# Kernel tuning notes

Hardware: AMD Instinct MI355X
Metric: run time of the kernel (lower is better)

The kernel has to match this reference:

```python
import jax, jax.numpy as jnp
import numpy as np

B, M, K, F_IN, H = 64, 1024, 16, 4, 64  # B graphs of M nodes each, k=16 neighbors


def _knn_idx(h):
    # h: [B, M, H] -> indices of K nearest neighbors (excluding self): [B, M, K]
    sq = jnp.sum(h * h, axis=-1)                                   # [B, M]
    d = sq[:, :, None] + sq[:, None, :] - 2.0 * jnp.einsum('bmf,bnf->bmn', h, h)
    d = jnp.where(jnp.eye(M, dtype=bool)[None], jnp.float32(jnp.inf), d)
    _, idx = jax.lax.top_k(-d, K)                                  # smallest distances
    return idx


def _edge_conv(h, w1, b1, w2, b2):
    # Dynamic-graph EdgeConv with max aggregation (PyG default):
    # msg = MLP(concat[x_i, x_j - x_i]); out_i = max_j msg
    idx = _knn_idx(h)                                              # [B, M, K]
    x_j = jax.vmap(lambda hb, ib: hb[ib])(h, idx)                  # [B, M, K, H]
    x_i = jnp.broadcast_to(h[:, :, None, :], x_j.shape)
    msg = jnp.concatenate([x_i, x_j - x_i], axis=-1)               # [B, M, K, 2H]
    msg = jax.nn.relu(msg @ w1 + b1) @ w2 + b2                     # [B, M, K, H]
    return jnp.max(msg, axis=2)                                    # [B, M, H]


def setup_inputs() -> dict:
    key = jax.random.key(0)
    ks = jax.random.split(key, 20)

    def lin(k, fi, fo):
        return jax.random.normal(k, (fi, fo), jnp.float32) / np.sqrt(fi)

    inp = {
        'x': jax.random.normal(ks[0], (B * M, F_IN), jnp.float32),
        'batch': jnp.repeat(jnp.arange(B, dtype=jnp.int64), M),
        # encoder: Linear(4,32) ReLU Linear(32,64) ReLU
        'enc_w1': lin(ks[1], F_IN, 32), 'enc_b1': jnp.zeros((32,), jnp.float32),
        'enc_w2': lin(ks[2], 32, H),    'enc_b2': jnp.zeros((H,), jnp.float32),
        # EdgeConv MLPs: Linear(128,64) ReLU Linear(64,64)
        'ec1_w1': lin(ks[3], 2 * H, H), 'ec1_b1': jnp.zeros((H,), jnp.float32),
        'ec1_w2': lin(ks[4], H, H),     'ec1_b2': jnp.zeros((H,), jnp.float32),
        'ec2_w1': lin(ks[5], 2 * H, H), 'ec2_b1': jnp.zeros((H,), jnp.float32),
        'ec2_w2': lin(ks[6], H, H),     'ec2_b2': jnp.zeros((H,), jnp.float32),
        # output MLP: Linear(64,32) ReLU Linear(32,1)
        'out_w1': lin(ks[7], H, 32),    'out_b1': jnp.zeros((32,), jnp.float32),
        'out_w2': lin(ks[8], 32, 1),    'out_b2': jnp.zeros((1,), jnp.float32),
    }
    return inp


def reference(x, batch, enc_w1, enc_b1, enc_w2, enc_b2,
              ec1_w1, ec1_b1, ec1_w2, ec1_b2,
              ec2_w1, ec2_b1, ec2_w2, ec2_b2,
              out_w1, out_b1, out_w2, out_b2):
    # batch is repeat(arange(B), M): equal-size graphs -> reshape into [B, M, .]
    h = jax.nn.relu(jax.nn.relu(x @ enc_w1 + enc_b1) @ enc_w2 + enc_b2)  # [N, 64]
    h = h.reshape(B, M, H)
    h = _edge_conv(h, ec1_w1, ec1_b1, ec1_w2, ec1_b2)
    h = _edge_conv(h, ec2_w1, ec2_b1, ec2_w2, ec2_b2)
    g = jnp.mean(h, axis=1)                                        # global_mean_pool -> [B, 64]
    out = jax.nn.relu(g @ out_w1 + out_b1) @ out_w2 + out_b2       # [B, 1]
    return out.reshape(-1)                                         # [B]
```

## Files before the change

### kernel.cpp

```cpp
#include <hip/hip_runtime.h>
#include <math.h>

#define B_ 64
#define M_ 1024
#define H_ 64
#define N_ (B_*M_)

typedef _Float16 half8 __attribute__((ext_vector_type(8)));
typedef float  floatx4 __attribute__((ext_vector_type(4)));

#define MFMA16(a,b,c) __builtin_amdgcn_mfma_f32_16x16x32_f16(a,b,c,0,0,0)
#define MED3(a,b,c)   __builtin_amdgcn_fmed3f(a,b,c)

__global__ __launch_bounds__(256) void enc_kernel(
    const float* __restrict__ x,
    const float* __restrict__ w1,
    const float* __restrict__ b1,
    const float* __restrict__ w2,
    const float* __restrict__ b2,
    float* __restrict__ h,
    _Float16* __restrict__ hhi,
    _Float16* __restrict__ hlo,
    float* __restrict__ sq)
{
    __shared__ float sw1[4*32];
    __shared__ float sb1[32];
    __shared__ float sw2[32*64];
    __shared__ float sb2[64];
    int t = threadIdx.x;
    for (int i = t; i < 128; i += 256) sw1[i] = w1[i];
    if (t < 32) sb1[t] = b1[t];
    for (int i = t; i < 2048; i += 256) sw2[i] = w2[i];
    if (t < 64) sb2[t] = b2[t];
    __syncthreads();
    int n = blockIdx.x * 256 + t;
    float4 xv = *(const float4*)(x + (size_t)n*4);
    float hid[32];
    #pragma unroll
    for (int o = 0; o < 32; ++o) {
        float a = sb1[o] + xv.x*sw1[0*32+o] + xv.y*sw1[1*32+o]
                        + xv.z*sw1[2*32+o] + xv.w*sw1[3*32+o];
        hid[o] = fmaxf(a, 0.f);
    }
    float* hout = h + (size_t)n*64;
    float sqa = 0.f;
    #pragma unroll 4
    for (int oc = 0; oc < 16; ++oc) {
        float4 acc = make_float4(sb2[oc*4+0], sb2[oc*4+1], sb2[oc*4+2], sb2[oc*4+3]);
        #pragma unroll
        for (int f = 0; f < 32; ++f) {
            float4 w = *(const float4*)(sw2 + f*64 + oc*4);
            float hv = hid[f];
            acc.x += hv*w.x; acc.y += hv*w.y; acc.z += hv*w.z; acc.w += hv*w.w;
        }
        acc.x = fmaxf(acc.x,0.f); acc.y = fmaxf(acc.y,0.f);
        acc.z = fmaxf(acc.z,0.f); acc.w = fmaxf(acc.w,0.f);
        *(float4*)(hout + oc*4) = acc;
        sqa += acc.x*acc.x + acc.y*acc.y + acc.z*acc.z + acc.w*acc.w;
        union { _Float16 f[4]; uint2 u; } Hh, Hl;
        Hh.f[0]=(_Float16)acc.x; Hh.f[1]=(_Float16)acc.y;
        Hh.f[2]=(_Float16)acc.z; Hh.f[3]=(_Float16)acc.w;
        Hl.f[0]=(_Float16)(acc.x-(float)Hh.f[0]); Hl.f[1]=(_Float16)(acc.y-(float)Hh.f[1]);
        Hl.f[2]=(_Float16)(acc.z-(float)Hh.f[2]); Hl.f[3]=(_Float16)(acc.w-(float)Hh.f[3]);
        *(uint2*)(hhi + (size_t)n*64 + oc*4) = Hh.u;
        *(uint2*)(hlo + (size_t)n*64 + oc*4) = Hl.u;
    }
    sq[n] = sqa;
}

__global__ __launch_bounds__(256) void convert_kernel(
    const float* __restrict__ h,
    _Float16* __restrict__ hhi, _Float16* __restrict__ hlo,
    float* __restrict__ sq)
{
    int t = threadIdx.x, lane = t & 63, w = t >> 6;
    int base = blockIdx.x * 64 + w * 16;
    for (int it = 0; it < 16; ++it) {
        int i = base + it;
        float v = h[(size_t)i*64 + lane];
        _Float16 hi = (_Float16)v;
        _Float16 lo = (_Float16)(v - (float)hi);
        hhi[(size_t)i*64 + lane] = hi;
        hlo[(size_t)i*64 + lane] = lo;
        float s = v*v;
        #pragma unroll
        for (int off = 1; off < 64; off <<= 1) s += __shfl_xor(s, off, 64);
        if (lane == 0) sq[i] = s;
    }
}

__global__ __launch_bounds__(256) void gemmA_kernel(
    const float* __restrict__ h,
    const float* __restrict__ w1,
    float* __restrict__ A)
{
    __shared__ float sw[64*64];
    int t = threadIdx.x;
    for (int idx = t; idx < 4096; idx += 256) sw[idx] = w1[4096 + idx];
    __syncthreads();
    int n = blockIdx.x * 256 + t;
    float4 hv[16];
    const float* src = h + (size_t)n*64;
    #pragma unroll
    for (int c = 0; c < 16; ++c) hv[c] = *(const float4*)(src + c*4);
    float* dst = A + (size_t)n*64;
    #pragma unroll 2
    for (int oc = 0; oc < 16; ++oc) {
        float4 acc = make_float4(0.f,0.f,0.f,0.f);
        #pragma unroll
        for (int f = 0; f < 64; ++f) {
            float xv = ((const float*)hv)[f];
            float4 w = *(const float4*)(sw + f*64 + oc*4);
            acc.x += xv*w.x; acc.y += xv*w.y; acc.z += xv*w.z; acc.w += xv*w.w;
        }
        *(float4*)(dst + oc*4) = acc;
    }
}

__global__ __launch_bounds__(256) void knn_kernel(
    const _Float16* __restrict__ hhi,
    const _Float16* __restrict__ hlo,
    const float* __restrict__ sqg,
    unsigned short* __restrict__ knn)
{
    __shared__ float D[4][64*33];
    __shared__ float sqS[1024];
    int t = threadIdx.x, lane = t & 63, w = t >> 6;
    int bi = blockIdx.x;
    int g  = (bi & 7) | ((bi >> 7) << 3);
    int qt = (bi >> 3) & 15;
    const _Float16* hhig = hhi + (size_t)g*M_*64;
    const _Float16* hlog = hlo + (size_t)g*M_*64;
    const float*    sqb  = sqg + (size_t)g*M_;
    ((float4*)sqS)[t] = ((const float4*)sqb)[t];

    int m16  = lane & 15;
    int koct = (lane >> 4) * 8;
    half8 Ahi[4][2], Alo[4][2];
    #pragma unroll
    for (int rb = 0; rb < 4; ++rb) {
        const _Float16* ph = hhig + (size_t)(qt*64 + rb*16 + m16)*64;
        const _Float16* pl = hlog + (size_t)(qt*64 + rb*16 + m16)*64;
        Ahi[rb][0] = *(const half8*)(ph + koct);
        Ahi[rb][1] = *(const half8*)(ph + 32 + koct);
        Alo[rb][0] = *(const half8*)(pl + koct);
        Alo[rb][1] = *(const half8*)(pl + 32 + koct);
    }
    float* Dw   = D[w];
    int    crow = (lane >> 4) * 4;
    float  bd[16];
    #pragma unroll
    for (int k = 0; k < 16; ++k) bd[k] = INFINITY;
    int cand0 = w*256;
    __syncthreads();
    float c1 = 1.f + sqS[qt*64 + lane];
    int selfc_all = qt*64 + lane;

    #pragma unroll
    for (int cc = 0; cc < 8; ++cc) {
        int cbase = cand0 + cc*32;
        half8 Bhi[2][2], Blo[2][2];
        #pragma unroll
        for (int cb = 0; cb < 2; ++cb) {
            const _Float16* ph = hhig + (size_t)(cbase + cb*16 + m16)*64;
            const _Float16* pl = hlog + (size_t)(cbase + cb*16 + m16)*64;
            Bhi[cb][0] = *(const half8*)(ph + koct);
            Bhi[cb][1] = *(const half8*)(ph + 32 + koct);
            Blo[cb][0] = *(const half8*)(pl + koct);
            Blo[cb][1] = *(const half8*)(pl + 32 + koct);
        }
        #pragma unroll
        for (int rb = 0; rb < 4; ++rb) {
            #pragma unroll
            for (int cb = 0; cb < 2; ++cb) {
                floatx4 acc = {0.f, 0.f, 0.f, 0.f};
                acc = MFMA16(Ahi[rb][0], Bhi[cb][0], acc);
                acc = MFMA16(Ahi[rb][1], Bhi[cb][1], acc);
                acc = MFMA16(Ahi[rb][0], Blo[cb][0], acc);
                acc = MFMA16(Ahi[rb][1], Blo[cb][1], acc);
                acc = MFMA16(Alo[rb][0], Bhi[cb][0], acc);
                acc = MFMA16(Alo[rb][1], Bhi[cb][1], acc);
                #pragma unroll
                for (int r = 0; r < 4; ++r)
                    Dw[(rb*16 + crow + r)*33 + cb*16 + m16] = acc[r];
            }
        }
        const float* drow = Dw + lane*33;
        int selfc = selfc_all - cbase;
        #pragma unroll
        for (int c8 = 0; c8 < 4; ++c8) {
            float sv[8], qv[8];
            #pragma unroll
            for (int j = 0; j < 8; ++j) {
                sv[j] = drow[c8*8 + j];
                qv[j] = sqS[cbase + c8*8 + j];
            }
            #pragma unroll
            for (int j = 0; j < 8; ++j) {
                int c = c8*8 + j;
                float s  = fmaf(-2.f, sv[j], qv[j]);
                float t2 = c1 + s;
                unsigned kb = (__float_as_uint(t2) & 0xFFFFFC00u)
                            | (unsigned)(cbase + c);
                float fk = __uint_as_float(kb);
                if (c == selfc) fk = INFINITY;
                float nb0 = fminf(bd[0], fk);
                #pragma unroll
                for (int k = 15; k >= 1; --k) bd[k] = MED3(fk, bd[k-1], bd[k]);
                bd[0] = nb0;
            }
        }
    }

    __syncthreads();
    float* md = &D[0][0];
    #pragma unroll
    for (int k = 0; k < 16; ++k) md[lane*65 + w*16 + k] = bd[k];
    __syncthreads();
    if (w == 0) {
        float b2[16];
        #pragma unroll
        for (int k = 0; k < 16; ++k) b2[k] = INFINITY;
        const float* mrow = md + lane*65;
        #pragma unroll
        for (int c8 = 0; c8 < 8; ++c8) {
            float sv[8];
            #pragma unroll
            for (int j = 0; j < 8; ++j) sv[j] = mrow[c8*8 + j];
            #pragma unroll
            for (int j = 0; j < 8; ++j) {
                float s = sv[j];
                float nb0 = fminf(b2[0], s);
                #pragma unroll
                for (int k = 15; k >= 1; --k) b2[k] = MED3(s, b2[k-1], b2[k]);
                b2[0] = nb0;
            }
        }
        union { unsigned short us[16]; uint4 v4[2]; } o;
        #pragma unroll
        for (int k = 0; k < 16; ++k)
            o.us[k] = (unsigned short)(__float_as_uint(b2[k]) & 1023u);
        size_t gq = (size_t)g*M_ + qt*64 + lane;
        uint4* dst = (uint4*)(knn + gq*16);
        dst[0] = o.v4[0];
        dst[1] = o.v4[1];
    }
}

__global__ __launch_bounds__(256) void edge_kernel(
    const float* __restrict__ h,
    const float* __restrict__ A,
    const unsigned short* __restrict__ knn,
    const float* __restrict__ w1,
    const float* __restrict__ b1,
    const float* __restrict__ w2,
    const float* __restrict__ b2,
    float* __restrict__ hout)
{
    __shared__ __align__(16) _Float16 wdf[16*64*8];
    __shared__ __align__(16) _Float16 w2f[16*64*8];
    float* CsB = (float*)w2f;
    int t = threadIdx.x;
    for (int u = t; u < 512; u += 256) {
        int ulane = u & 63, nt = u >> 7, ks = (u >> 6) & 1;
        int n = nt*16 + (ulane & 15);
        int kbase = ks*32 + ((ulane >> 4) * 8);
        int fh = (((nt*2+ks)*2+0)*64 + ulane)*8;
        int fl = (((nt*2+ks)*2+1)*64 + ulane)*8;
        #pragma unroll
        for (int j = 0; j < 8; ++j) {
            int k = kbase + j;
            float vd = w1[k*64+n] - w1[4096 + k*64+n];
            _Float16 dh = (_Float16)vd;
            wdf[fh+j] = dh;
            wdf[fl+j] = (_Float16)(vd - (float)dh);
            float v2 = w2[k*64+n];
            _Float16 h2 = (_Float16)v2;
            w2f[fh+j] = h2;
            w2f[fl+j] = (_Float16)(v2 - (float)h2);
        }
    }
    __syncthreads();
    int lane = t & 63, wid = t >> 6;
    int m16 = lane & 15, gid = lane >> 4;
    int koct = gid*8, crow = gid*4;
    int bi = blockIdx.x;
    int g  = (bi & 7) | ((bi >> 7) << 3);
    int qt = (bi >> 3) & 15;
    int i0 = g*M_ + qt*64 + wid*16;
    const float* Ab = A + (size_t)g*M_*H_;

    half8 W2r[4][2][2];
    #pragma unroll
    for (int nt = 0; nt < 4; ++nt)
        #pragma unroll
        for (int ks = 0; ks < 2; ++ks)
            #pragma unroll
            for (int p = 0; p < 2; ++p)
                W2r[nt][ks][p] = *(const half8*)&w2f[(((nt*2+ks)*2+p)*64+lane)*8];

    float b1v[4];
    #pragma unroll
    for (int nt = 0; nt < 4; ++nt) b1v[nt] = b1[nt*16+m16];
    float b2v = b2[gid*16+m16];
    __syncthreads();

    half8 Hh[2], Hl[2];
    #pragma unroll
    for (int ks = 0; ks < 2; ++ks) {
        const float* hp = h + (size_t)(i0+m16)*64 + ks*32 + koct;
        float4 v0 = *(const float4*)hp;
        float4 v1 = *(const float4*)(hp+4);
        float va[8] = {v0.x,v0.y,v0.z,v0.w,v1.x,v1.y,v1.z,v1.w};
        #pragma unroll
        for (int j = 0; j < 8; ++j) {
            _Float16 hi = (_Float16)va[j];
            Hh[ks][j] = hi;
            Hl[ks][j] = (_Float16)(va[j]-(float)hi);
        }
    }
    #pragma unroll
    for (int nt = 0; nt < 4; ++nt) {
        floatx4 acc = {b1v[nt], b1v[nt], b1v[nt], b1v[nt]};
        #pragma unroll
        for (int ks = 0; ks < 2; ++ks) {
            half8 wh = *(const half8*)&wdf[(((nt*2+ks)*2+0)*64+lane)*8];
            half8 wl = *(const half8*)&wdf[(((nt*2+ks)*2+1)*64+lane)*8];
            acc = MFMA16(Hh[ks], wh, acc);
            acc = MFMA16(Hh[ks], wl, acc);
            acc = MFMA16(Hl[ks], wh, acc);
        }
        #pragma unroll
        for (int r = 0; r < 4; ++r)
            CsB[((wid*16) + crow + r)*64 + nt*16 + m16] = acc[r];
    }
    __syncthreads();

    const unsigned short* knb = knn + (size_t)i0*16;
    #pragma unroll 2
    for (int nn = 0; nn < 16; ++nn) {
        int j = knb[nn*16 + m16];
        const float* Ap = Ab + (size_t)j*64;
        half8 Mh[2], Ml[2];
        #pragma unroll
        for (int ks = 0; ks < 2; ++ks) {
            float4 a0 = *(const float4*)(Ap + ks*32 + koct);
            float4 a1 = *(const float4*)(Ap + ks*32 + koct + 4);
            const float* cp = &CsB[(wid*16 + nn)*64 + ks*32 + koct];
            float4 c0 = *(const float4*)cp;
            float4 c1 = *(const float4*)(cp+4);
            float mv[8] = {
                fmaxf(a0.x+c0.x,0.f), fmaxf(a0.y+c0.y,0.f),
                fmaxf(a0.z+c0.z,0.f), fmaxf(a0.w+c0.w,0.f),
                fmaxf(a1.x+c1.x,0.f), fmaxf(a1.y+c1.y,0.f),
                fmaxf(a1.z+c1.z,0.f), fmaxf(a1.w+c1.w,0.f)};
            #pragma unroll
            for (int jj = 0; jj < 8; ++jj) {
                _Float16 hi = (_Float16)mv[jj];
                Mh[ks][jj] = hi;
                Ml[ks][jj] = (_Float16)(mv[jj]-(float)hi);
            }
        }
        floatx4 acc[4];
        #pragma unroll
        for (int nt = 0; nt < 4; ++nt) {
            acc[nt] = (floatx4){0.f,0.f,0.f,0.f};
            #pragma unroll
            for (int ks = 0; ks < 2; ++ks) {
                acc[nt] = MFMA16(Mh[ks], W2r[nt][ks][0], acc[nt]);
                acc[nt] = MFMA16(Mh[ks], W2r[nt][ks][1], acc[nt]);
                acc[nt] = MFMA16(Ml[ks], W2r[nt][ks][0], acc[nt]);
            }
        }
        float om[4];
        #pragma unroll
        for (int nt = 0; nt < 4; ++nt) {
            float mr = fmaxf(fmaxf(acc[nt][0], acc[nt][1]),
                             fmaxf(acc[nt][2], acc[nt][3]));
            mr = fmaxf(mr, __shfl_xor(mr, 16, 64));
            mr = fmaxf(mr, __shfl_xor(mr, 32, 64));
            om[nt] = mr;
        }
        float val = (gid == 0) ? om[0] : (gid == 1) ? om[1]
                  : (gid == 2) ? om[2] : om[3];
        hout[(size_t)(i0+nn)*64 + gid*16 + m16] = val + b2v;
    }
}

__global__ __launch_bounds__(256) void pool_kernel(
    const float* __restrict__ h,
    const float* __restrict__ w1,
    const float* __restrict__ b1,
    const float* __restrict__ w2,
    const float* __restrict__ b2,
    float* __restrict__ out)
{
    __shared__ float part[4][64];
    __shared__ float g[64];
    __shared__ float hid[32];
    int t = threadIdx.x;
    int o = t & 63, p = t >> 6;
    int b = blockIdx.x;
    const float* hb = h + (size_t)b*M_*H_;
    float s = 0.f;
    for (int m = p; m < M_; m += 4) s += hb[(size_t)m*64 + o];
    part[p][o] = s;
    __syncthreads();
    if (t < 64) g[t] = (part[0][t] + part[1][t] + part[2][t] + part[3][t]) * (1.f/M_);
    __syncthreads();
    if (t < 32) {
        float a = b1[t];
        for (int f = 0; f < 64; ++f) a += g[f] * w1[f*32 + t];
        hid[t] = fmaxf(a, 0.f);
    }
    __syncthreads();
    if (t == 0) {
        float a = b2[0];
        for (int f = 0; f < 32; ++f) a += hid[f] * w2[f];
        out[b] = a;
    }
}

extern "C" void kernel_launch(void* const* d_in, const int* in_sizes, int n_in,
                              void* d_out, int out_size, void* d_ws, size_t ws_size,
                              hipStream_t stream)
{
    (void)in_sizes; (void)n_in; (void)out_size; (void)ws_size;
    const float* x      = (const float*)d_in[0];
    const float* enc_w1 = (const float*)d_in[2];
    const float* enc_b1 = (const float*)d_in[3];
    const float* enc_w2 = (const float*)d_in[4];
    const float* enc_b2 = (const float*)d_in[5];
    const float* ec1_w1 = (const float*)d_in[6];
    const float* ec1_b1 = (const float*)d_in[7];
    const float* ec1_w2 = (const float*)d_in[8];
    const float* ec1_b2 = (const float*)d_in[9];
    const float* ec2_w1 = (const float*)d_in[10];
    const float* ec2_b1 = (const float*)d_in[11];
    const float* ec2_w2 = (const float*)d_in[12];
    const float* ec2_b2 = (const float*)d_in[13];
    const float* out_w1 = (const float*)d_in[14];
    const float* out_b1 = (const float*)d_in[15];
    const float* out_w2 = (const float*)d_in[16];
    const float* out_b2 = (const float*)d_in[17];

    char* ws = (char*)d_ws;
    float*          h   = (float*)(ws);
    char*           r2  = ws + (size_t)N_*64*4;
    _Float16*       hhi = (_Float16*)r2;
    _Float16*       hlo = (_Float16*)(r2 + (size_t)N_*64*2);
    float*          A   = (float*)r2;
    unsigned short* idx = (unsigned short*)(ws + (size_t)N_*64*4*2);
    float*          sq  = (float*)(ws + (size_t)N_*64*4*2 + (size_t)N_*16*2);

    enc_kernel<<<N_/256, 256, 0, stream>>>(x, enc_w1, enc_b1, enc_w2, enc_b2,
                                           h, hhi, hlo, sq);
    knn_kernel <<<B_*16, 256, 0, stream>>>(hhi, hlo, sq, idx);
    gemmA_kernel<<<N_/256, 256, 0, stream>>>(h, ec1_w1, A);
    edge_kernel<<<N_/64, 256, 0, stream>>>(h, A, idx, ec1_w1, ec1_b1, ec1_w2, ec1_b2, h);
    convert_kernel<<<N_/64, 256, 0, stream>>>(h, hhi, hlo, sq);
    knn_kernel <<<B_*16, 256, 0, stream>>>(hhi, hlo, sq, idx);
    gemmA_kernel<<<N_/256, 256, 0, stream>>>(h, ec2_w1, A);
    edge_kernel<<<N_/64, 256, 0, stream>>>(h, A, idx, ec2_w1, ec2_b1, ec2_w2, ec2_b2, h);
    pool_kernel<<<B_, 256, 0, stream>>>(h, out_w1, out_b1, out_w2, out_b2, (float*)d_out);
}
```

Baseline: 420.0 us.

## Restructure kNN kernel with double-buffered LDS candidate tiles and MFMA-direct selection

Rewrites the kNN distance/top-k kernel so that each wave owns 16 query rows and all 1024 candidates are streamed through double-buffered, XOR-swizzled shared-memory tiles of 16 rows. Global loads are prefetched two tiles ahead. The MFMA results are consumed straight from registers for top-k insertion instead of being written to and reread from an LDS distance matrix. Each lane now keeps a partial top-16 over a strided subset of candidates, and these are merged as before. The change adds a launch-bounds occupancy hint of 4 and many block barriers per tile, which may cost synchronization overhead.

```diff
diff --git a/kernel.cpp b/kernel.cpp
--- a/kernel.cpp
+++ b/kernel.cpp
@@ -117,14 +117,17 @@
     }
 }
 
-__global__ __launch_bounds__(256) void knn_kernel(
+__global__ __launch_bounds__(256, 4) void knn_kernel(
     const _Float16* __restrict__ hhi,
     const _Float16* __restrict__ hlo,
     const float* __restrict__ sqg,
     unsigned short* __restrict__ knn)
 {
-    __shared__ float D[4][64*33];
-    __shared__ float sqS[1024];
+    __shared__ __align__(16) _Float16 bufH[2][16*64];
+    __shared__ __align__(16) _Float16 bufL[2][16*64];
+    __shared__ __align__(16) float sqS[1024];
+    __shared__ float md[64*65];
+
     int t = threadIdx.x, lane = t & 63, w = t >> 6;
     int bi = blockIdx.x;
     int g  = (bi & 7) | ((bi >> 7) << 3);
@@ -132,90 +135,98 @@
     const _Float16* hhig = hhi + (size_t)g*M_*64;
     const _Float16* hlog = hlo + (size_t)g*M_*64;
     const float*    sqb  = sqg + (size_t)g*M_;
+
     ((float4*)sqS)[t] = ((const float4*)sqb)[t];
 
-    int m16  = lane & 15;
-    int koct = (lane >> 4) * 8;
-    half8 Ahi[4][2], Alo[4][2];
-    #pragma unroll
-    for (int rb = 0; rb < 4; ++rb) {
-        const _Float16* ph = hhig + (size_t)(qt*64 + rb*16 + m16)*64;
-        const _Float16* pl = hlog + (size_t)(qt*64 + rb*16 + m16)*64;
-        Ahi[rb][0] = *(const half8*)(ph + koct);
-        Ahi[rb][1] = *(const half8*)(ph + 32 + koct);
-        Alo[rb][0] = *(const half8*)(pl + koct);
-        Alo[rb][1] = *(const half8*)(pl + 32 + koct);
-    }
-    float* Dw   = D[w];
-    int    crow = (lane >> 4) * 4;
-    float  bd[16];
+    int m16 = lane & 15, gid = lane >> 4;
+    int crow = gid*4, koct = gid*8;
+    int sw = m16 & 7;
+
+    int rr = (w & 1)*8 + (lane >> 3);
+    int gl = lane & 7;
+    int pp = gl ^ (rr & 7);
+    const _Float16* srcb = (w < 2 ? hhig : hlog) + rr*64 + gl*8;
+    int dsto = rr*64 + pp*8;
+    _Float16* db0 = (w < 2 ? bufH[0] : bufL[0]) + dsto;
+    _Float16* db1 = (w < 2 ? bufH[1] : bufL[1]) + dsto;
+
+    half8 Qh0, Qh1, Ql0, Ql1;
+    {
+        const _Float16* ph = hhig + (size_t)(qt*64 + w*16 + m16)*64;
+        const _Float16* pl = hlog + (size_t)(qt*64 + w*16 + m16)*64;
+        Qh0 = *(const half8*)(ph + koct);
+        Qh1 = *(const half8*)(ph + 32 + koct);
+        Ql0 = *(const half8*)(pl + koct);
+        Ql1 = *(const half8*)(pl + 32 + koct);
+    }
+
+    float bd[16];
     #pragma unroll
     for (int k = 0; k < 16; ++k) bd[k] = INFINITY;
-    int cand0 = w*256;
-    __syncthreads();
-    float c1 = 1.f + sqS[qt*64 + lane];
-    int selfc_all = qt*64 + lane;
-
-    #pragma unroll
-    for (int cc = 0; cc < 8; ++cc) {
-        int cbase = cand0 + cc*32;
-        half8 Bhi[2][2], Blo[2][2];
-        #pragma unroll
-        for (int cb = 0; cb < 2; ++cb) {
-            const _Float16* ph = hhig + (size_t)(cbase + cb*16 + m16)*64;
-            const _Float16* pl = hlog + (size_t)(cbase + cb*16 + m16)*64;
-            Bhi[cb][0] = *(const half8*)(ph + koct);
-            Bhi[cb][1] = *(const half8*)(ph + 32 + koct);
-            Blo[cb][0] = *(const half8*)(pl + koct);
-            Blo[cb][1] = *(const half8*)(pl + 32 + koct);
-        }
-        #pragma unroll
-        for (int rb = 0; rb < 4; ++rb) {
-            #pragma unroll
-            for (int cb = 0; cb < 2; ++cb) {
-                floatx4 acc = {0.f, 0.f, 0.f, 0.f};
-                acc = MFMA16(Ahi[rb][0], Bhi[cb][0], acc);
-                acc = MFMA16(Ahi[rb][1], Bhi[cb][1], acc);
-                acc = MFMA16(Ahi[rb][0], Blo[cb][0], acc);
-                acc = MFMA16(Ahi[rb][1], Blo[cb][1], acc);
-                acc = MFMA16(Alo[rb][0], Bhi[cb][0], acc);
-                acc = MFMA16(Alo[rb][1], Bhi[cb][1], acc);
-                #pragma unroll
-                for (int r = 0; r < 4; ++r)
-                    Dw[(rb*16 + crow + r)*33 + cb*16 + m16] = acc[r];
-            }
-        }
-        const float* drow = Dw + lane*33;
-        int selfc = selfc_all - cbase;
-        #pragma unroll
-        for (int c8 = 0; c8 < 4; ++c8) {
-            float sv[8], qv[8];
-            #pragma unroll
-            for (int j = 0; j < 8; ++j) {
-                sv[j] = drow[c8*8 + j];
-                qv[j] = sqS[cbase + c8*8 + j];
-            }
-            #pragma unroll
-            for (int j = 0; j < 8; ++j) {
-                int c = c8*8 + j;
-                float s  = fmaf(-2.f, sv[j], qv[j]);
-                float t2 = c1 + s;
-                unsigned kb = (__float_as_uint(t2) & 0xFFFFFC00u)
-                            | (unsigned)(cbase + c);
-                float fk = __uint_as_float(kb);
-                if (c == selfc) fk = INFINITY;
-                float nb0 = fminf(bd[0], fk);
-                #pragma unroll
-                for (int k = 15; k >= 1; --k) bd[k] = MED3(fk, bd[k-1], bd[k]);
-                bd[0] = nb0;
-            }
-        }
-    }
-
-    __syncthreads();
-    float* md = &D[0][0];
-    #pragma unroll
-    for (int k = 0; k < 16; ++k) md[lane*65 + w*16 + k] = bd[k];
+
+    int t_self = qt*4 + w;
+
+    float4 ldA = *(const float4*)(srcb);
+    float4 ldB = *(const float4*)(srcb + 1024);
+    *(float4*)db0 = ldA;
+    ldA = *(const float4*)(srcb + 2*1024);
+    __syncthreads();
+
+    float c1 = 1.f + sqS[qt*64 + w*16 + m16];
+
+    int o0 = m16*64 + ((gid ^ sw) * 8);
+    int o1 = o0 ^ 32;
+
+    auto compute = [&](int T, const _Float16* bh, const _Float16* bl) {
+        half8 Ah0 = *(const half8*)(bh + o0);
+        half8 Ah1 = *(const half8*)(bh + o1);
+        half8 Al0 = *(const half8*)(bl + o0);
+        half8 Al1 = *(const half8*)(bl + o1);
+        floatx4 acc = {0.f, 0.f, 0.f, 0.f};
+        acc = MFMA16(Ah0, Qh0, acc);
+        acc = MFMA16(Ah1, Qh1, acc);
+        acc = MFMA16(Ah0, Ql0, acc);
+        acc = MFMA16(Ah1, Ql1, acc);
+        acc = MFMA16(Al0, Qh0, acc);
+        acc = MFMA16(Al1, Qh1, acc);
+        float4 sqv = *(const float4*)(sqS + T*16 + crow);
+        unsigned cid = (unsigned)(T*16 + crow);
+        bool st = (T == t_self);
+        #pragma unroll
+        for (int r = 0; r < 4; ++r) {
+            float s  = fmaf(-2.f, acc[r], (&sqv.x)[r]);
+            float t2 = c1 + s;
+            unsigned kb = (__float_as_uint(t2) & 0xFFFFFC00u) | (cid + r);
+            float fk = __uint_as_float(kb);
+            if (st && (crow + r) == m16) fk = INFINITY;
+            float nb0 = fminf(bd[0], fk);
+            #pragma unroll
+            for (int k = 15; k >= 1; --k) bd[k] = MED3(fk, bd[k-1], bd[k]);
+            bd[0] = nb0;
+        }
+    };
+
+    #pragma unroll 1
+    for (int T = 0; T < 64; T += 2) {
+        __builtin_amdgcn_s_barrier();
+        *(float4*)db1 = ldB;
+        ldB = *(const float4*)(srcb + (size_t)((T+3)&63)*1024);
+        asm volatile("s_waitcnt lgkmcnt(0)" ::: "memory");
+        __builtin_amdgcn_s_barrier();
+        __builtin_amdgcn_sched_barrier(0);
+        compute(T, bufH[0], bufL[0]);
+        __builtin_amdgcn_s_barrier();
+        *(float4*)db0 = ldA;
+        ldA = *(const float4*)(srcb + (size_t)((T+4)&63)*1024);
+        asm volatile("s_waitcnt lgkmcnt(0)" ::: "memory");
+        __builtin_amdgcn_s_barrier();
+        __builtin_amdgcn_sched_barrier(0);
+        compute(T+1, bufH[1], bufL[1]);
+    }
+
+    int qrow = w*16 + m16;
+    #pragma unroll
+    for (int k = 0; k < 16; ++k) md[qrow*65 + gid*16 + k] = bd[k];
     __syncthreads();
     if (w == 0) {
         float b2[16];
```

New measurement: 413.5 us. About the same (-1.6%).
